# Optimization experiments

Measured on AMD Instinct MI355X. Metric: run time of the kernel, lower is better.

## Reference

```python
import jax, jax.numpy as jnp
import numpy as np
import math

B, C, TC, H, W = 8, 256, 512, 48, 48
EPS = 1e-6

def setup_inputs() -> dict:
    key = jax.random.key(0)
    kx, kt, kq, kk, kv = jax.random.split(key, 5)
    x = jax.random.normal(kx, (B, C, H, W), dtype=jnp.float32)
    token = jax.random.normal(kt, (B, TC, H, W), dtype=jnp.float32)
    # xavier_uniform for 1x1 conv weights [out, in]
    def xavier(k, fan_out, fan_in):
        a = math.sqrt(6.0 / (fan_in + fan_out))
        return jax.random.uniform(k, (fan_out, fan_in), dtype=jnp.float32, minval=-a, maxval=a)
    Wq = xavier(kq, C, C)
    Wk = xavier(kk, C, TC)
    Wv = xavier(kv, C, TC)
    alpha = jnp.float32(0.5)  # nonzero so the attention path affects the output
    return {"x": x, "token": token, "Wq": Wq, "Wk": Wk, "Wv": Wv, "alpha": alpha}

def reference(x, token, Wq, Wk, Wv, alpha):
    # 1x1 convs == per-pixel GEMMs over the channel dim
    q = jnp.einsum('oc,bchw->bohw', Wq, x)       # [B,C,H,W]
    k = jnp.einsum('oc,bchw->bohw', Wk, token)   # [B,C,H,W]
    v = jnp.einsum('oc,bchw->bohw', Wv, token)   # [B,C,H,W]
    b, c, h, w = q.shape
    n = h * w
    qf = q.reshape(b, c, n).transpose(0, 2, 1)   # [B,N,C]
    kf = k.reshape(b, c, n)                      # [B,C,N]
    vf = v.reshape(b, c, n).transpose(0, 2, 1)   # [B,N,C]
    # cosine normalization over the channel dim (F.normalize with eps clamp)
    qn = qf / jnp.maximum(jnp.linalg.norm(qf, axis=-1, keepdims=True), EPS)
    kn = kf / jnp.maximum(jnp.linalg.norm(kf, axis=1, keepdims=True), EPS)
    attn = jnp.einsum('bnc,bcm->bnm', qn, kn) / math.sqrt(c)  # [B,N,N]
    attn = jax.nn.softmax(attn, axis=-1)
    out = jnp.einsum('bnm,bmc->bnc', attn, vf)   # [B,N,C]
    out = out.transpose(0, 2, 1).reshape(b, c, h, w)
    return x + alpha * out
```

## Files before the change

kernel.cpp:

```cpp
#include <hip/hip_runtime.h>

#define B_   8
#define C_   256
#define TC_  512
#define HW_  2304
#define EPS_ 1e-6f

typedef __bf16 bf16_t;
typedef __bf16 bf16x8 __attribute__((ext_vector_type(8)));
typedef __bf16 bf16x4_t __attribute__((ext_vector_type(4)));
typedef float  f32x4 __attribute__((ext_vector_type(4)));
typedef unsigned int  u32;
typedef unsigned int  u32x2 __attribute__((ext_vector_type(2)));
typedef unsigned int  u32x4 __attribute__((ext_vector_type(4)));
typedef long long     i64;
typedef unsigned char u8;

__device__ __forceinline__ void g2l16(const void* g, void* l) {
    __builtin_amdgcn_global_load_lds(
        (const __attribute__((address_space(1))) unsigned int*)g,
        (__attribute__((address_space(3))) unsigned int*)l, 16, 0, 0);
}

__device__ __forceinline__ u8 to_fp8(float v) {
    return (u8)(__builtin_amdgcn_cvt_pk_fp8_f32(v, v, 0, false) & 0xff);
}

__global__ __launch_bounds__(256)
void wfrag_kernel(const float* __restrict__ wq, const float* __restrict__ wk,
                  const float* __restrict__ wv,
                  bf16_t* __restrict__ oq, bf16_t* __restrict__ ok,
                  bf16_t* __restrict__ ov)
{
    const int fid = blockIdx.x * 4 + (threadIdx.x >> 6);
    const int lane = threadIdx.x & 63;
    const int l16 = lane & 15, quad = lane >> 4;

    const float* src; bf16_t* dst; int cin, f;
    if (fid < 128)      { src = wq; dst = oq; cin = C_;  f = fid; }
    else if (fid < 384) { src = wk; dst = ok; cin = TC_; f = fid - 128; }
    else                { src = wv; dst = ov; cin = TC_; f = fid - 384; }
    const int nks = cin / 32;
    const int ot = f / nks, ks = f % nks;

    const float* s = src + (size_t)(ot * 16 + l16) * cin + ks * 32 + quad * 8;
    float4 a = *(const float4*)(s);
    float4 b = *(const float4*)(s + 4);
    bf16x8 o;
    o[0] = (__bf16)a.x; o[1] = (__bf16)a.y; o[2] = (__bf16)a.z; o[3] = (__bf16)a.w;
    o[4] = (__bf16)b.x; o[5] = (__bf16)b.y; o[6] = (__bf16)b.z; o[7] = (__bf16)b.w;
    *(bf16x8*)(dst + (size_t)f * 512 + lane * 8) = o;
}

template<int CIN, bool DO_V>
__global__ __launch_bounds__(256, 4)
void convqkv_kernel(const float* __restrict__ X, const bf16_t* __restrict__ Wa,
                    const bf16_t* __restrict__ Wvp, u8* __restrict__ outA,
                    u8* __restrict__ outV)
{
    const int bid = blockIdx.x;
    const int b  = bid & 7;
    const int n0 = (bid >> 3) * 16;
    const int tid = threadIdx.x;
    const int wv = tid >> 6;
    const int lane = tid & 63;
    const int quad = lane >> 4, l16 = lane & 15;
    const int NKS = CIN / 32;

    __shared__ bf16_t T[16][CIN + 8];
    __shared__ float ssp[4][16];

    {
        const float* Xb = X + (size_t)b * CIN * HW_ + n0;
        const int cl = tid >> 2;
        const int n4 = (tid & 3) * 4;
#pragma unroll
        for (int cp = 0; cp < CIN; cp += 64) {
            float4 v = *(const float4*)(Xb + (size_t)(cp + cl) * HW_ + n4);
            T[n4 + 0][cp + cl] = (__bf16)v.x;
            T[n4 + 1][cp + cl] = (__bf16)v.y;
            T[n4 + 2][cp + cl] = (__bf16)v.z;
            T[n4 + 3][cp + cl] = (__bf16)v.w;
        }
    }
    __syncthreads();

    bf16x8 af[CIN / 32];
#pragma unroll
    for (int ks = 0; ks < CIN / 32; ks++)
        af[ks] = *(const bf16x8*)(&T[l16][ks * 32 + quad * 8]);

    const int ot0 = wv * 4;

    f32x4 accK[4];
#pragma unroll
    for (int p = 0; p < 4; p++) accK[p] = (f32x4){0.f, 0.f, 0.f, 0.f};
    {
        const bf16_t* wbase = Wa + ((size_t)ot0 * NKS) * 512 + lane * 8;
#pragma unroll
        for (int ks = 0; ks < CIN / 32; ks++)
#pragma unroll
            for (int p = 0; p < 4; p++) {
                bf16x8 bw = *(const bf16x8*)(wbase + (size_t)(p * NKS + ks) * 512);
                accK[p] = __builtin_amdgcn_mfma_f32_16x16x32_bf16(af[ks], bw, accK[p], 0, 0, 0);
            }
    }

    {
        float ssr[4];
#pragma unroll
        for (int r = 0; r < 4; r++) {
            float ss = accK[0][r] * accK[0][r] + accK[1][r] * accK[1][r]
                     + accK[2][r] * accK[2][r] + accK[3][r] * accK[3][r];
            ss += __shfl_xor(ss, 1);
            ss += __shfl_xor(ss, 2);
            ss += __shfl_xor(ss, 4);
            ss += __shfl_xor(ss, 8);
            ssr[r] = ss;
        }
        if (l16 == 0) {
#pragma unroll
            for (int r = 0; r < 4; r++) ssp[wv][quad * 4 + r] = ssr[r];
        }
    }

    f32x4 accV[4];
    if (DO_V) {
#pragma unroll
        for (int p = 0; p < 4; p++) accV[p] = (f32x4){0.f, 0.f, 0.f, 0.f};
        const bf16_t* wbase = Wvp + ((size_t)ot0 * NKS) * 512 + lane * 8;
#pragma unroll
        for (int ks = 0; ks < CIN / 32; ks++)
#pragma unroll
            for (int p = 0; p < 4; p++) {
                bf16x8 aw = *(const bf16x8*)(wbase + (size_t)(p * NKS + ks) * 512);
                accV[p] = __builtin_amdgcn_mfma_f32_16x16x32_bf16(aw, af[ks], accV[p], 0, 0, 0);
            }
    }

    __syncthreads();

    float scale[4];
#pragma unroll
    for (int r = 0; r < 4; r++) {
        int px = quad * 4 + r;
        float s = ssp[0][px] + ssp[1][px] + ssp[2][px] + ssp[3][px];
        scale[r] = 1.0f / fmaxf(sqrtf(s), EPS_);
    }
    {
        u8* oa = outA + ((size_t)b * HW_ + n0 + quad * 4) * C_ + l16;
#pragma unroll
        for (int p = 0; p < 4; p++)
#pragma unroll
            for (int r = 0; r < 4; r++)
                oa[(size_t)r * C_ + (ot0 + p) * 16] = to_fp8(accK[p][r] * scale[r]);
    }

    if (DO_V) {
#pragma unroll
        for (int p = 0; p < 4; p++)
#pragma unroll
            for (int r = 0; r < 4; r++)
                outV[((size_t)b * C_ + (ot0 + p) * 16 + quad * 4 + r) * HW_ + n0 + l16]
                    = to_fp8(accV[p][r]);
    }
}

__global__ __launch_bounds__(256, 2)
void attn_part_kernel(const u8* __restrict__ q8, const u8* __restrict__ k8,
                      const u8* __restrict__ v8,
                      bf16_t* __restrict__ Opart, float* __restrict__ lpart,
                      int tilesPerSplit, int JS)
{
    const int bid = blockIdx.x;
    const int b   = bid & 7;
    const int rr  = bid >> 3;
    const int js  = rr % JS;
    const int mt  = rr / JS;
    const int wv   = threadIdx.x >> 6;
    const int lane = threadIdx.x & 63;
    const int quad = lane >> 4;
    const int l16  = lane & 15;
    const int row0 = mt * 128 + wv * 32;
    const int jbase = js * tilesPerSplit * 32;

    const u8* qb = q8 + (size_t)b * HW_ * C_;
    const u8* kb = k8 + (size_t)b * HW_ * C_;
    const u8* vb = v8 + (size_t)b * C_ * HW_;

    __shared__ u8 Kbuf[2][8192];
    __shared__ u8 Vbuf[2][8192];
    __shared__ u8 Pt[4][1536];

    i64 aq0[8], aq1[8];
    {
        const u8* r0 = qb + (size_t)(row0 + l16) * C_ + quad * 8;
        const u8* r1 = r0 + 16 * C_;
#pragma unroll
        for (int t = 0; t < 8; t++) {
            aq0[t] = *(const i64*)(r0 + t * 32);
            aq1[t] = *(const i64*)(r1 + t * 32);
        }
    }

    f32x4 O0[16], O1[16];
#pragma unroll
    for (int i = 0; i < 16; i++) {
        O0[i] = (f32x4){0.f, 0.f, 0.f, 0.f};
        O1[i] = (f32x4){0.f, 0.f, 0.f, 0.f};
    }
    float lsum0[4] = {0.f, 0.f, 0.f, 0.f};
    float lsum1[4] = {0.f, 0.f, 0.f, 0.f};

    const int kj = lane & 31;
    const int kh = lane >> 5;
    const int vg = lane & 1;
    const int vc = lane >> 1;

#define STAGE(bufi, j0g)                                                       \
    {                                                                          \
        _Pragma("unroll")                                                      \
        for (int p = 0; p < 2; p++) {                                          \
            int i = wv * 2 + p;                                                \
            int s = i * 2 + kh;                                                \
            g2l16(kb + (size_t)((j0g) + kj) * C_ + s * 16,                     \
                  &Kbuf[bufi][i * 1024]);                                      \
        }                                                                      \
        _Pragma("unroll")                                                      \
        for (int p = 0; p < 2; p++) {                                          \
            int i = wv * 2 + p;                                                \
            int c = i * 32 + vc;                                               \
            g2l16(vb + (size_t)c * HW_ + (j0g) + vg * 16,                      \
                  &Vbuf[bufi][i * 1024]);                                      \
        }                                                                      \
    }

    STAGE(0, jbase)

    u8* pw = &Pt[wv][0];
    const int koff = (quad >> 1) * 512 + l16 * 16 + (quad & 1) * 8;
    const u32 sel = (quad < 2) ? 0x06040200u : 0x07050301u;

    for (int tt = 0; tt < tilesPerSplit; tt++) {
        __syncthreads();
        if (tt + 1 < tilesPerSplit) STAGE((tt + 1) & 1, jbase + (tt + 1) * 32)

        const u8* Kb = Kbuf[tt & 1];
        const u8* Vb = Vbuf[tt & 1];

        f32x4 s00 = (f32x4){0.f,0.f,0.f,0.f}, s01 = (f32x4){0.f,0.f,0.f,0.f};
        f32x4 s10 = (f32x4){0.f,0.f,0.f,0.f}, s11 = (f32x4){0.f,0.f,0.f,0.f};
#pragma unroll
        for (int t = 0; t < 8; t++) {
            i64 bk0 = *(const i64*)(Kb + t * 1024 + koff);
            i64 bk1 = *(const i64*)(Kb + t * 1024 + koff + 256);
            s00 = __builtin_amdgcn_mfma_f32_16x16x32_fp8_fp8(aq0[t], bk0, s00, 0, 0, 0);
            s01 = __builtin_amdgcn_mfma_f32_16x16x32_fp8_fp8(aq0[t], bk1, s01, 0, 0, 0);
            s10 = __builtin_amdgcn_mfma_f32_16x16x32_fp8_fp8(aq1[t], bk0, s10, 0, 0, 0);
            s11 = __builtin_amdgcn_mfma_f32_16x16x32_fp8_fp8(aq1[t], bk1, s11, 0, 0, 0);
        }
#pragma unroll
        for (int r = 0; r < 4; r++) {
            float p00 = __expf(s00[r] * 0.0625f), p01 = __expf(s01[r] * 0.0625f);
            float p10 = __expf(s10[r] * 0.0625f), p11 = __expf(s11[r] * 0.0625f);
            lsum0[r] += p00 + p01;
            lsum1[r] += p10 + p11;
            u32 w0 = __builtin_amdgcn_cvt_pk_fp8_f32(p00, p01, 0, false);
            u32 w1 = __builtin_amdgcn_cvt_pk_fp8_f32(p10, p11, 0, false);
            int ro = (quad * 4 + r) * 48 + l16 * 2;
            *(short*)(pw + ro)       = (short)w0;
            *(short*)(pw + 768 + ro) = (short)w1;
        }
        i64 ap0, ap1;
        {
            u32x4 d = *(const u32x4*)(pw + l16 * 48 + (quad & 1) * 16);
            u32 lo = __builtin_amdgcn_perm(d[1], d[0], sel);
            u32 hi = __builtin_amdgcn_perm(d[3], d[2], sel);
            ap0 = ((i64)hi << 32) | (i64)lo;
            u32x4 e = *(const u32x4*)(pw + 768 + l16 * 48 + (quad & 1) * 16);
            lo = __builtin_amdgcn_perm(e[1], e[0], sel);
            hi = __builtin_amdgcn_perm(e[3], e[2], sel);
            ap1 = ((i64)hi << 32) | (i64)lo;
        }
#pragma unroll
        for (int ct = 0; ct < 16; ct++) {
            i64 bv = *(const i64*)(Vb + ct * 512 + l16 * 32 + quad * 8);
            O0[ct] = __builtin_amdgcn_mfma_f32_16x16x32_fp8_fp8(ap0, bv, O0[ct], 0, 0, 0);
            O1[ct] = __builtin_amdgcn_mfma_f32_16x16x32_fp8_fp8(ap1, bv, O1[ct], 0, 0, 0);
        }
    }

#pragma unroll
    for (int r = 0; r < 4; r++) {
        float t0 = lsum0[r], t1 = lsum1[r];
        t0 += __shfl_xor(t0, 1); t0 += __shfl_xor(t0, 2);
        t0 += __shfl_xor(t0, 4); t0 += __shfl_xor(t0, 8);
        t1 += __shfl_xor(t1, 1); t1 += __shfl_xor(t1, 2);
        t1 += __shfl_xor(t1, 4); t1 += __shfl_xor(t1, 8);
        lsum0[r] = t0; lsum1[r] = t1;
    }
    float* lp = lpart + (size_t)(js * B_ + b) * HW_;
    if (l16 == 0) {
        float4 a0; a0.x = lsum0[0]; a0.y = lsum0[1]; a0.z = lsum0[2]; a0.w = lsum0[3];
        float4 a1; a1.x = lsum1[0]; a1.y = lsum1[1]; a1.z = lsum1[2]; a1.w = lsum1[3];
        *(float4*)(lp + row0 + quad * 4)      = a0;
        *(float4*)(lp + row0 + 16 + quad * 4) = a1;
    }
    bf16_t* op = Opart + (size_t)(js * B_ + b) * C_ * HW_;
#pragma unroll
    for (int ct = 0; ct < 16; ct++) {
        int c = ct * 16 + l16;
        bf16x4_t v0, v1;
        v0[0] = (__bf16)O0[ct][0]; v0[1] = (__bf16)O0[ct][1];
        v0[2] = (__bf16)O0[ct][2]; v0[3] = (__bf16)O0[ct][3];
        v1[0] = (__bf16)O1[ct][0]; v1[1] = (__bf16)O1[ct][1];
        v1[2] = (__bf16)O1[ct][2]; v1[3] = (__bf16)O1[ct][3];
        *(bf16x4_t*)(op + (size_t)c * HW_ + row0 + quad * 4)      = v0;
        *(bf16x4_t*)(op + (size_t)c * HW_ + row0 + 16 + quad * 4) = v1;
    }
#undef STAGE
}

__global__ __launch_bounds__(256)
void epilogue_kernel(const float* __restrict__ x, const bf16_t* __restrict__ Opart,
                     const float* __restrict__ lpart, const float* __restrict__ alphaPtr,
                     float* __restrict__ out, int JS)
{
    const float a = *alphaPtr;
    const size_t S = (size_t)B_ * C_ * HW_;
    size_t flat = ((size_t)blockIdx.x * 256 + threadIdx.x) * 4;
    int bc = (int)(flat / HW_);
    int n  = (int)(flat % HW_);
    int b  = bc >> 8;
    float4 xv = *(const float4*)(x + flat);
    float s0 = 0.f, s1 = 0.f, s2 = 0.f, s3 = 0.f;
    float l0 = 0.f, l1 = 0.f, l2 = 0.f, l3 = 0.f;
    for (int js = 0; js < JS; js++) {
        bf16x4_t ov = *(const bf16x4_t*)(Opart + (size_t)js * S + flat);
        s0 += (float)ov[0]; s1 += (float)ov[1];
        s2 += (float)ov[2]; s3 += (float)ov[3];
        float4 lv = *(const float4*)(lpart + (size_t)(js * B_ + b) * HW_ + n);
        l0 += lv.x; l1 += lv.y; l2 += lv.z; l3 += lv.w;
    }
    float4 r;
    r.x = xv.x + a * s0 / l0;
    r.y = xv.y + a * s1 / l1;
    r.z = xv.z + a * s2 / l2;
    r.w = xv.w + a * s3 / l3;
    *(float4*)(out + flat) = r;
}

extern "C" void kernel_launch(void* const* d_in, const int* in_sizes, int n_in,
                              void* d_out, int out_size, void* d_ws, size_t ws_size,
                              hipStream_t stream)
{
    (void)in_sizes; (void)n_in; (void)out_size;
    const float* x     = (const float*)d_in[0];
    const float* token = (const float*)d_in[1];
    const float* Wq    = (const float*)d_in[2];
    const float* Wk    = (const float*)d_in[3];
    const float* Wv    = (const float*)d_in[4];
    const float* alpha = (const float*)d_in[5];
    float* out = (float*)d_out;

    const size_t S = (size_t)B_ * HW_ * C_;

    int JS = 8;
    for (;;) {
        size_t need = (12 + 2 * (size_t)JS) * S
                    + (size_t)JS * B_ * HW_ * 4 + (size_t)B_ * HW_ * 4;
        if (need <= ws_size || JS == 1) break;
        JS >>= 1;
    }
    const int tilesPerSplit = (HW_ / 32) / JS;

    char* ws = (char*)d_ws;
    bf16_t* WqL   = (bf16_t*)(ws + 6 * S);
    bf16_t* WkL   = WqL + (size_t)C_ * C_;
    bf16_t* WvL   = WkL + (size_t)C_ * TC_;
    u8*     q8    = (u8*)(ws + 7 * S);
    u8*     k8    = (u8*)(ws + 8 * S);
    u8*     v8    = (u8*)(ws + 9 * S);
    bf16_t* Opart = (bf16_t*)(ws + 12 * S);
    float*  lpart = (float*)(ws + (12 + 2 * (size_t)JS) * S);

    wfrag_kernel<<<dim3(160), dim3(256), 0, stream>>>(Wq, Wk, Wv, WqL, WkL, WvL);
    convqkv_kernel<C_,  false><<<dim3(B_ * HW_ / 16), dim3(256), 0, stream>>>(x,     WqL, nullptr, q8, nullptr);
    convqkv_kernel<TC_, true ><<<dim3(B_ * HW_ / 16), dim3(256), 0, stream>>>(token, WkL, WvL,     k8, v8);
    attn_part_kernel<<<dim3(JS * B_ * (HW_ / 128)), dim3(256), 0, stream>>>(q8, k8, v8, Opart, lpart, tilesPerSplit, JS);
    epilogue_kernel<<<dim3((int)(S / 1024)), dim3(256), 0, stream>>>(x, Opart, lpart, alpha, out, JS);
}
```

Before: 242.6 us.

## Preload whole K/V split slab into LDS and split PV by channel across waves

The attention kernel now loads the entire K and V slab for its split (9 tiles, about 147KB of LDS) up front instead of double-buffering one tile at a time, and hardcodes JS=8. The P·V stage is reorganised so that each wave owns 64 output channels for all 128 rows, reading every wave's P tile from shared memory. This is meant to remove per-tile global-load latency and reduce redundant V reads from LDS. In exchange it needs extra barriers per tile, allows only one block per CU, and drops the workspace-size fallback.

```diff
diff --git a/kernel.cpp b/kernel.cpp
--- a/kernel.cpp
+++ b/kernel.cpp
@@ -5,13 +5,14 @@
 #define TC_  512
 #define HW_  2304
 #define EPS_ 1e-6f
+#define JS_  8
+#define TPS_ 9
 
 typedef __bf16 bf16_t;
 typedef __bf16 bf16x8 __attribute__((ext_vector_type(8)));
 typedef __bf16 bf16x4_t __attribute__((ext_vector_type(4)));
 typedef float  f32x4 __attribute__((ext_vector_type(4)));
 typedef unsigned int  u32;
-typedef unsigned int  u32x2 __attribute__((ext_vector_type(2)));
 typedef unsigned int  u32x4 __attribute__((ext_vector_type(4)));
 typedef long long     i64;
 typedef unsigned char u8;
@@ -166,31 +167,45 @@
     }
 }
 
-__global__ __launch_bounds__(256, 2)
+__global__ __launch_bounds__(256, 1)
 void attn_part_kernel(const u8* __restrict__ q8, const u8* __restrict__ k8,
                       const u8* __restrict__ v8,
-                      bf16_t* __restrict__ Opart, float* __restrict__ lpart,
-                      int tilesPerSplit, int JS)
+                      bf16_t* __restrict__ Opart, float* __restrict__ lpart)
 {
     const int bid = blockIdx.x;
     const int b   = bid & 7;
     const int rr  = bid >> 3;
-    const int js  = rr % JS;
-    const int mt  = rr / JS;
+    const int js  = rr % JS_;
+    const int mtb = rr / JS_;
     const int wv   = threadIdx.x >> 6;
     const int lane = threadIdx.x & 63;
     const int quad = lane >> 4;
     const int l16  = lane & 15;
-    const int row0 = mt * 128 + wv * 32;
-    const int jbase = js * tilesPerSplit * 32;
+    const int row0 = mtb * 128 + wv * 32;
+    const int jbase = js * (TPS_ * 32);
 
     const u8* qb = q8 + (size_t)b * HW_ * C_;
     const u8* kb = k8 + (size_t)b * HW_ * C_;
     const u8* vb = v8 + (size_t)b * C_ * HW_;
 
-    __shared__ u8 Kbuf[2][8192];
-    __shared__ u8 Vbuf[2][8192];
-    __shared__ u8 Pt[4][1536];
+    __shared__ u8 Kslab[TPS_ * 8192];
+    __shared__ u8 Vslab[TPS_ * 8192];
+    __shared__ u8 Psh[8 * 768];
+
+    const int kj = lane & 31, kh = lane >> 5;
+    const int vg = lane & 1,  vc = lane >> 1;
+    for (int t = 0; t < 18; t++) {
+        int ii = wv * 18 + t;
+        int tt = ii >> 3, i = ii & 7;
+        g2l16(kb + (size_t)(jbase + tt * 32 + kj) * C_ + (i * 2 + kh) * 16,
+              Kslab + ii * 1024);
+    }
+    for (int t = 0; t < 18; t++) {
+        int jj = wv * 18 + t;
+        int tt = jj >> 3, i2 = jj & 7;
+        g2l16(vb + (size_t)(i2 * 32 + vc) * HW_ + jbase + tt * 32 + vg * 16,
+              Vslab + jj * 1024);
+    }
 
     i64 aq0[8], aq1[8];
     {
@@ -203,50 +218,24 @@
         }
     }
 
-    f32x4 O0[16], O1[16];
-#pragma unroll
-    for (int i = 0; i < 16; i++) {
-        O0[i] = (f32x4){0.f, 0.f, 0.f, 0.f};
-        O1[i] = (f32x4){0.f, 0.f, 0.f, 0.f};
-    }
+    f32x4 O[8][4];
+#pragma unroll
+    for (int m = 0; m < 8; m++)
+#pragma unroll
+        for (int c = 0; c < 4; c++) O[m][c] = (f32x4){0.f, 0.f, 0.f, 0.f};
     float lsum0[4] = {0.f, 0.f, 0.f, 0.f};
     float lsum1[4] = {0.f, 0.f, 0.f, 0.f};
 
-    const int kj = lane & 31;
-    const int kh = lane >> 5;
-    const int vg = lane & 1;
-    const int vc = lane >> 1;
-
-#define STAGE(bufi, j0g)                                                       \
-    {                                                                          \
-        _Pragma("unroll")                                                      \
-        for (int p = 0; p < 2; p++) {                                          \
-            int i = wv * 2 + p;                                                \
-            int s = i * 2 + kh;                                                \
-            g2l16(kb + (size_t)((j0g) + kj) * C_ + s * 16,                     \
-                  &Kbuf[bufi][i * 1024]);                                      \
-        }                                                                      \
-        _Pragma("unroll")                                                      \
-        for (int p = 0; p < 2; p++) {                                          \
-            int i = wv * 2 + p;                                                \
-            int c = i * 32 + vc;                                               \
-            g2l16(vb + (size_t)c * HW_ + (j0g) + vg * 16,                      \
-                  &Vbuf[bufi][i * 1024]);                                      \
-        }                                                                      \
-    }
-
-    STAGE(0, jbase)
-
-    u8* pw = &Pt[wv][0];
+    __syncthreads();
+
+    u8* pw = Psh + wv * 1536;
     const int koff = (quad >> 1) * 512 + l16 * 16 + (quad & 1) * 8;
     const u32 sel = (quad < 2) ? 0x06040200u : 0x07050301u;
-
-    for (int tt = 0; tt < tilesPerSplit; tt++) {
-        __syncthreads();
-        if (tt + 1 < tilesPerSplit) STAGE((tt + 1) & 1, jbase + (tt + 1) * 32)
-
-        const u8* Kb = Kbuf[tt & 1];
-        const u8* Vb = Vbuf[tt & 1];
+    const int vcol = (wv * 64 + l16) * 32 + quad * 8;
+
+    for (int tt = 0; tt < TPS_; tt++) {
+        const u8* Kb = Kslab + tt * 8192;
+        const u8* Vb = Vslab + tt * 8192;
 
         f32x4 s00 = (f32x4){0.f,0.f,0.f,0.f}, s01 = (f32x4){0.f,0.f,0.f,0.f};
         f32x4 s10 = (f32x4){0.f,0.f,0.f,0.f}, s11 = (f32x4){0.f,0.f,0.f,0.f};
@@ -271,23 +260,26 @@
             *(short*)(pw + ro)       = (short)w0;
             *(short*)(pw + 768 + ro) = (short)w1;
         }
-        i64 ap0, ap1;
-        {
-            u32x4 d = *(const u32x4*)(pw + l16 * 48 + (quad & 1) * 16);
+        __syncthreads();
+
+        i64 ap[8];
+#pragma unroll
+        for (int mt = 0; mt < 8; mt++) {
+            u32x4 d = *(const u32x4*)(Psh + mt * 768 + l16 * 48 + (quad & 1) * 16);
             u32 lo = __builtin_amdgcn_perm(d[1], d[0], sel);
             u32 hi = __builtin_amdgcn_perm(d[3], d[2], sel);
-            ap0 = ((i64)hi << 32) | (i64)lo;
-            u32x4 e = *(const u32x4*)(pw + 768 + l16 * 48 + (quad & 1) * 16);
-            lo = __builtin_amdgcn_perm(e[1], e[0], sel);
-            hi = __builtin_amdgcn_perm(e[3], e[2], sel);
-            ap1 = ((i64)hi << 32) | (i64)lo;
-        }
-#pragma unroll
-        for (int ct = 0; ct < 16; ct++) {
-            i64 bv = *(const i64*)(Vb + ct * 512 + l16 * 32 + quad * 8);
-            O0[ct] = __builtin_amdgcn_mfma_f32_16x16x32_fp8_fp8(ap0, bv, O0[ct], 0, 0, 0);
-            O1[ct] = __builtin_amdgcn_mfma_f32_16x16x32_fp8_fp8(ap1, bv, O1[ct], 0, 0, 0);
-        }
+            ap[mt] = ((i64)hi << 32) | (i64)lo;
+        }
+        i64 bv[4];
+#pragma unroll
+        for (int ct = 0; ct < 4; ct++)
+            bv[ct] = *(const i64*)(Vb + vcol + ct * 512);
+#pragma unroll
+        for (int mt = 0; mt < 8; mt++)
+#pragma unroll
+            for (int ct = 0; ct < 4; ct++)
+                O[mt][ct] = __builtin_amdgcn_mfma_f32_16x16x32_fp8_fp8(ap[mt], bv[ct], O[mt][ct], 0, 0, 0);
+        __syncthreads();
     }
 
 #pragma unroll
@@ -306,19 +298,18 @@
         *(float4*)(lp + row0 + quad * 4)      = a0;
         *(float4*)(lp + row0 + 16 + quad * 4) = a1;
     }
+
     bf16_t* op = Opart + (size_t)(js * B_ + b) * C_ * HW_;
 #pragma unroll
-    for (int ct = 0; ct < 16; ct++) {
-        int c = ct * 16 + l16;
-        bf16x4_t v0, v1;
-        v0[0] = (__bf16)O0[ct][0]; v0[1] = (__bf16)O0[ct][1];
-        v0[2] = (__bf16)O0[ct][2]; v0[3] = (__bf16)O0[ct][3];
-        v1[0] = (__bf16)O1[ct][0]; v1[1] = (__bf16)O1[ct][1];
-        v1[2] = (__bf16)O1[ct][2]; v1[3] = (__bf16)O1[ct][3];
-        *(bf16x4_t*)(op + (size_t)c * HW_ + row0 + quad * 4)      = v0;
-        *(bf16x4_t*)(op + (size_t)c * HW_ + row0 + 16 + quad * 4) = v1;
-    }
-#undef STAGE
+    for (int mt = 0; mt < 8; mt++)
+#pragma unroll
+        for (int ct = 0; ct < 4; ct++) {
+            int c = wv * 64 + ct * 16 + l16;
+            bf16x4_t v0;
+            v0[0] = (__bf16)O[mt][ct][0]; v0[1] = (__bf16)O[mt][ct][1];
+            v0[2] = (__bf16)O[mt][ct][2]; v0[3] = (__bf16)O[mt][ct][3];
+            *(bf16x4_t*)(op + (size_t)c * HW_ + mtb * 128 + mt * 16 + quad * 4) = v0;
+        }
 }
 
 __global__ __launch_bounds__(256)
@@ -354,7 +345,7 @@
                               void* d_out, int out_size, void* d_ws, size_t ws_size,
                               hipStream_t stream)
 {
-    (void)in_sizes; (void)n_in; (void)out_size;
+    (void)in_sizes; (void)n_in; (void)out_size; (void)ws_size;
     const float* x     = (const float*)d_in[0];
     const float* token = (const float*)d_in[1];
     const float* Wq    = (const float*)d_in[2];
@@ -364,15 +355,6 @@
     float* out = (float*)d_out;
 
     const size_t S = (size_t)B_ * HW_ * C_;
-
-    int JS = 8;
-    for (;;) {
-        size_t need = (12 + 2 * (size_t)JS) * S
-                    + (size_t)JS * B_ * HW_ * 4 + (size_t)B_ * HW_ * 4;
-        if (need <= ws_size || JS == 1) break;
-        JS >>= 1;
-    }
-    const int tilesPerSplit = (HW_ / 32) / JS;
 
     char* ws = (char*)d_ws;
     bf16_t* WqL   = (bf16_t*)(ws + 6 * S);
@@ -382,11 +364,11 @@
     u8*     k8    = (u8*)(ws + 8 * S);
     u8*     v8    = (u8*)(ws + 9 * S);
     bf16_t* Opart = (bf16_t*)(ws + 12 * S);
-    float*  lpart = (float*)(ws + (12 + 2 * (size_t)JS) * S);
+    float*  lpart = (float*)(ws + (12 + 2 * (size_t)JS_) * S);
 
     wfrag_kernel<<<dim3(160), dim3(256), 0, stream>>>(Wq, Wk, Wv, WqL, WkL, WvL);
     convqkv_kernel<C_,  false><<<dim3(B_ * HW_ / 16), dim3(256), 0, stream>>>(x,     WqL, nullptr, q8, nullptr);
     convqkv_kernel<TC_, true ><<<dim3(B_ * HW_ / 16), dim3(256), 0, stream>>>(token, WkL, WvL,     k8, v8);
-    attn_part_kernel<<<dim3(JS * B_ * (HW_ / 128)), dim3(256), 0, stream>>>(q8, k8, v8, Opart, lpart, tilesPerSplit, JS);
-    epilogue_kernel<<<dim3((int)(S / 1024)), dim3(256), 0, stream>>>(x, Opart, lpart, alpha, out, JS);
-}
+    attn_part_kernel<<<dim3(JS_ * B_ * (HW_ / 128)), dim3(256), 0, stream>>>(q8, k8, v8, Opart, lpart);
+    epilogue_kernel<<<dim3((int)(S / 1024)), dim3(256), 0, stream>>>(x, Opart, lpart, alpha, out, JS_);
+}
```

Result: slower. 264.5 us (+9.0%).
